# Kernel optimization log

Measured on AMD Instinct MI355X. Metric: run time of the kernel, lower is better.

The kernel has to match this reference:

```python
import jax, jax.numpy as jnp
import numpy as np

N, IN_DIM, KEY_DIM, K, VAL_DIM = 100000, 512, 100, 8, 64


def setup_inputs() -> dict:
    key = jax.random.key(0)
    ks = jax.random.split(key, 7)
    s = 0.02
    return {
        "x": jax.random.normal(ks[0], (N, IN_DIM), dtype=jnp.float32),
        "Wk": jax.random.normal(ks[1], (KEY_DIM, IN_DIM), dtype=jnp.float32) * s,
        "bk": jax.random.normal(ks[2], (KEY_DIM,), dtype=jnp.float32) * s,
        "Wq": jax.random.normal(ks[3], (K, KEY_DIM), dtype=jnp.float32) * s,
        "bq": jax.random.normal(ks[4], (K,), dtype=jnp.float32) * s,
        "Wv": jax.random.normal(ks[5], (VAL_DIM, IN_DIM), dtype=jnp.float32) * s,
        "bv": jax.random.normal(ks[6], (VAL_DIM,), dtype=jnp.float32) * s,
    }


def reference(x, Wk, bk, Wq, bq, Wv, bv):
    # torch.nn.Linear: y = x @ W.T + b
    key = x @ Wk.T + bk                  # [N, key_dim]
    val = x @ Wv.T + bv                  # [N, val_dim]
    que = key @ Wq.T + bq                # [N, k]
    # att_norm == 'softmax': per-sample softmax over the k groups
    w = jax.nn.softmax(que, axis=-1)     # [N, k]
    # per-sample outer product w_i^T @ val_i -> [N, k, val_dim]
    x_group = w[:, :, None] * val[:, None, :]
    return x_group
```

## Files before the change

kernel.cpp:

```cpp
#include <hip/hip_runtime.h>

#define NROWS 100000
#define IN_DIM 512

typedef __attribute__((ext_vector_type(8))) short short8;
typedef __attribute__((ext_vector_type(4))) float f32x4;
typedef unsigned int u32;
typedef const __attribute__((address_space(1))) u32* gptr_t;
typedef __attribute__((address_space(3))) u32* lptr_t;

__device__ inline unsigned short f2bf(float f) {
    union { float f; unsigned u; } v; v.f = f;
    unsigned u = v.u;
    return (unsigned short)((u + 0x7FFFu + ((u >> 16) & 1u)) >> 16);
}

__global__ void qg_prepack(const float* __restrict__ Wk, const float* __restrict__ bk,
                           const float* __restrict__ Wq, const float* __restrict__ bq,
                           const float* __restrict__ Wv,
                           unsigned short* __restrict__ Bp, float* __restrict__ qb) {
    int id = blockIdx.x * 256 + threadIdx.x;
    if (id < 8) {
        float s = bq[id];
        #pragma unroll 4
        for (int j = 0; j < 100; ++j) s += Wq[id * 100 + j] * bk[j];
        qb[id] = s;
    }
    if (id >= 5120) return;
    int lane = id & 63;
    int ks = (id >> 6) & 15;
    int t = id >> 10;
    int c = t * 16 + (lane & 15);
    int kk = ks * 32 + (lane >> 4) * 8;
    short8 pk;
    #pragma unroll
    for (int e = 0; e < 8; ++e) {
        int k2 = kk + e;
        float w;
        if (c < 64) {
            w = Wv[c * IN_DIM + k2];
        } else if (c < 72) {
            float s = 0.f;
            #pragma unroll 4
            for (int j = 0; j < 100; ++j) s += Wq[(c - 64) * 100 + j] * Wk[j * IN_DIM + k2];
            w = s;
        } else {
            w = 0.f;
        }
        pk[e] = (short)f2bf(w);
    }
    ((short8*)Bp)[id] = pk;
}

__global__ __launch_bounds__(128, 1) void qg_main(const float* __restrict__ x,
                                                  const float* __restrict__ bv,
                                                  const unsigned short* __restrict__ Bp,
                                                  const float* __restrict__ qb,
                                                  float* __restrict__ out) {
    __shared__ float smem[36864];
    const int tid = threadIdx.x;
    const int w = tid >> 6;
    const int lane = tid & 63;
    const int g = lane >> 4;
    const int cl = lane & 15;
    const int rowbase = (blockIdx.x * 2 + w) * 16;

    float* Bls = smem;
    float* tile = smem + 20480 + w * 8192;

    float bvr[4];
    #pragma unroll
    for (int t = 0; t < 4; ++t) bvr[t] = bv[t * 16 + cl];
    float qbr = qb[cl & 7];
    asm volatile("s_waitcnt vmcnt(0)" ::: "memory");

    #pragma unroll
    for (int j = 0; j < 40; ++j) {
        const int slot = w * 2560 + j * 64;
        const char* src = (const char*)Bp + ((size_t)(slot + lane)) * 16;
        __builtin_amdgcn_global_load_lds((gptr_t)(const void*)src,
                                         (lptr_t)(void*)(Bls + (size_t)slot * 4), 16, 0, 0);
    }
    __builtin_amdgcn_sched_barrier(0);

    #pragma unroll
    for (int i = 0; i < 32; ++i) {
        const int row = i >> 1;
        const int c = (((i & 1) * 64) + lane) ^ (row & 7);
        const float* src = x + (size_t)(rowbase + row) * IN_DIM + c * 4;
        __builtin_amdgcn_global_load_lds((gptr_t)(const void*)src,
                                         (lptr_t)(void*)(tile + i * 256), 16, 0, 0);
    }
    __builtin_amdgcn_sched_barrier(0);

    asm volatile("s_waitcnt vmcnt(32)" ::: "memory");
    __builtin_amdgcn_s_barrier();
    asm volatile("s_waitcnt vmcnt(0)" ::: "memory");
    __builtin_amdgcn_sched_barrier(0);

    f32x4 acc[5];
    #pragma unroll
    for (int t = 0; t < 5; ++t) acc[t] = (f32x4){0.f, 0.f, 0.f, 0.f};
    const float4* t4 = (const float4*)tile;
    const short8* b8 = (const short8*)Bls;

    #pragma unroll
    for (int s = 0; s < 16; ++s) {
        const int c0 = (s * 8 + g * 2)     ^ (cl & 7);
        const int c1 = (s * 8 + g * 2 + 1) ^ (cl & 7);
        float4 f0 = t4[cl * 128 + c0];
        float4 f1 = t4[cl * 128 + c1];
        short8 af;
        af[0] = (short)f2bf(f0.x); af[1] = (short)f2bf(f0.y);
        af[2] = (short)f2bf(f0.z); af[3] = (short)f2bf(f0.w);
        af[4] = (short)f2bf(f1.x); af[5] = (short)f2bf(f1.y);
        af[6] = (short)f2bf(f1.z); af[7] = (short)f2bf(f1.w);
        #pragma unroll
        for (int t = 0; t < 5; ++t)
            acc[t] = __builtin_amdgcn_mfma_f32_16x16x32_bf16(af, b8[(t * 16 + s) * 64 + lane], acc[t], 0, 0, 0);
    }

    asm volatile("s_waitcnt lgkmcnt(0)" ::: "memory");
    float (*vld)[68] = (float(*)[68])tile;
    float (*wld)[8]  = (float(*)[8])(tile + 16 * 68);
    #pragma unroll
    for (int t = 0; t < 4; ++t) {
        #pragma unroll
        for (int r = 0; r < 4; ++r)
            vld[g * 4 + r][t * 16 + cl] = acc[t][r] + bvr[t];
    }
    if (cl < 8) {
        #pragma unroll
        for (int r = 0; r < 4; ++r)
            wld[g * 4 + r][cl] = acc[4][r] + qbr;
    }
    asm volatile("s_waitcnt lgkmcnt(0)" ::: "memory");

    if (lane < 16) {
        float q[8];
        float m = -1e30f;
        #pragma unroll
        for (int k = 0; k < 8; ++k) { q[k] = wld[lane][k]; m = fmaxf(m, q[k]); }
        float ssum = 0.f;
        #pragma unroll
        for (int k = 0; k < 8; ++k) { q[k] = __expf(q[k] - m); ssum += q[k]; }
        float inv = 1.f / ssum;
        #pragma unroll
        for (int k = 0; k < 8; ++k) wld[lane][k] = q[k] * inv;
    }
    asm volatile("s_waitcnt lgkmcnt(0)" ::: "memory");

    f32x4* outp = (f32x4*)out + (size_t)rowbase * 128;
    #pragma unroll
    for (int it = 0; it < 32; ++it) {
        int idx = it * 64 + lane;
        int row = idx >> 7;
        int j = idx & 127;
        float wgt = wld[row][j >> 4];
        float4 vv = *(const float4*)&vld[row][(j & 15) * 4];
        f32x4 o;
        o[0] = wgt * vv.x; o[1] = wgt * vv.y; o[2] = wgt * vv.z; o[3] = wgt * vv.w;
        __builtin_nontemporal_store(o, &outp[(size_t)row * 128 + j]);
    }
}

extern "C" void kernel_launch(void* const* d_in, const int* in_sizes, int n_in,
                              void* d_out, int out_size, void* d_ws, size_t ws_size,
                              hipStream_t stream) {
    const float* x  = (const float*)d_in[0];
    const float* Wk = (const float*)d_in[1];
    const float* bk = (const float*)d_in[2];
    const float* Wq = (const float*)d_in[3];
    const float* bq = (const float*)d_in[4];
    const float* Wv = (const float*)d_in[5];
    const float* bv = (const float*)d_in[6];
    float* out = (float*)d_out;

    unsigned short* Bp = (unsigned short*)d_ws;
    float* qb = (float*)((char*)d_ws + 81920);

    qg_prepack<<<20, 256, 0, stream>>>(Wk, bk, Wq, bq, Wv, Bp, qb);
    qg_main<<<3125, 128, 0, stream>>>(x, bv, Bp, qb, out);
}
```

Baseline: 120.9 us.

## Make main kernel persistent with atomic tile scheduling and a five-slot load ring

Replaces the one-shot grid of 3125 two-wave blocks with 256 persistent four-wave blocks. Each wave pulls 16-row tiles from a global atomic counter that the prepack kernel resets. x is streamed through a per-wave five-slot LDS ring of 32-column chunks with counted vmcnt waits, so loads for the next chunks and the next tile overlap the MFMA work and the epilogue stores. The packed weights are loaded into LDS once per block instead of once per small block. In exchange the kernel needs an atomic per tile, has an intricate hand-tuned wait-count schedule, and its occupancy is limited to one large block per CU.

```diff
diff --git a/kernel.cpp b/kernel.cpp
--- a/kernel.cpp
+++ b/kernel.cpp
@@ -2,6 +2,7 @@
 
 #define NROWS 100000
 #define IN_DIM 512
+#define NTILES 6250
 
 typedef __attribute__((ext_vector_type(8))) short short8;
 typedef __attribute__((ext_vector_type(4))) float f32x4;
@@ -18,7 +19,8 @@
 __global__ void qg_prepack(const float* __restrict__ Wk, const float* __restrict__ bk,
                            const float* __restrict__ Wq, const float* __restrict__ bq,
                            const float* __restrict__ Wv,
-                           unsigned short* __restrict__ Bp, float* __restrict__ qb) {
+                           unsigned short* __restrict__ Bp, float* __restrict__ qb,
+                           u32* __restrict__ ctr) {
     int id = blockIdx.x * 256 + threadIdx.x;
     if (id < 8) {
         float s = bq[id];
@@ -26,6 +28,7 @@
         for (int j = 0; j < 100; ++j) s += Wq[id * 100 + j] * bk[j];
         qb[id] = s;
     }
+    if (id == 8) *ctr = 0u;
     if (id >= 5120) return;
     int lane = id & 63;
     int ks = (id >> 6) & 15;
@@ -52,21 +55,20 @@
     ((short8*)Bp)[id] = pk;
 }
 
-__global__ __launch_bounds__(128, 1) void qg_main(const float* __restrict__ x,
+__global__ __launch_bounds__(256, 1) void qg_main(const float* __restrict__ x,
                                                   const float* __restrict__ bv,
                                                   const unsigned short* __restrict__ Bp,
                                                   const float* __restrict__ qb,
+                                                  u32* __restrict__ ctr,
                                                   float* __restrict__ out) {
-    __shared__ float smem[36864];
+    __shared__ float Bls[20480];
+    __shared__ float ring[4][2560];
+    __shared__ float epi[4][1216];
     const int tid = threadIdx.x;
     const int w = tid >> 6;
     const int lane = tid & 63;
     const int g = lane >> 4;
     const int cl = lane & 15;
-    const int rowbase = (blockIdx.x * 2 + w) * 16;
-
-    float* Bls = smem;
-    float* tile = smem + 20480 + w * 8192;
 
     float bvr[4];
     #pragma unroll
@@ -74,94 +76,151 @@
     float qbr = qb[cl & 7];
     asm volatile("s_waitcnt vmcnt(0)" ::: "memory");
 
+    int t0 = 0, t1 = 0;
+    if (lane == 0) { t0 = (int)atomicAdd(ctr, 1u); t1 = (int)atomicAdd(ctr, 1u); }
+    int cur = __shfl(t0, 0);
+    int nxt = __shfl(t1, 0);
+
     #pragma unroll
-    for (int j = 0; j < 40; ++j) {
-        const int slot = w * 2560 + j * 64;
-        const char* src = (const char*)Bp + ((size_t)(slot + lane)) * 16;
-        __builtin_amdgcn_global_load_lds((gptr_t)(const void*)src,
-                                         (lptr_t)(void*)(Bls + (size_t)slot * 4), 16, 0, 0);
-    }
-    __builtin_amdgcn_sched_barrier(0);
-
-    #pragma unroll
-    for (int i = 0; i < 32; ++i) {
-        const int row = i >> 1;
-        const int c = (((i & 1) * 64) + lane) ^ (row & 7);
-        const float* src = x + (size_t)(rowbase + row) * IN_DIM + c * 4;
-        __builtin_amdgcn_global_load_lds((gptr_t)(const void*)src,
-                                         (lptr_t)(void*)(tile + i * 256), 16, 0, 0);
-    }
-    __builtin_amdgcn_sched_barrier(0);
-
-    asm volatile("s_waitcnt vmcnt(32)" ::: "memory");
+    for (int j = 0; j < 20; ++j) {
+        int s16 = w * 1280 + j * 64;
+        __builtin_amdgcn_global_load_lds(
+            (gptr_t)(const void*)((const char*)Bp + ((size_t)s16 + lane) * 16),
+            (lptr_t)(void*)(Bls + (size_t)s16 * 4), 16, 0, 0);
+    }
+
+    auto issue_chunk = [&](int rb, int st, int slot) {
+        #pragma unroll
+        for (int l = 0; l < 2; ++l) {
+            int S16 = l * 64 + lane;
+            int row = S16 >> 3;
+            int c = (S16 & 7) ^ (row & 7);
+            const float* src = x + (size_t)(rb + row) * IN_DIM + st * 32 + c * 4;
+            __builtin_amdgcn_global_load_lds((gptr_t)(const void*)src,
+                (lptr_t)(void*)(ring[w] + slot * 512 + l * 256), 16, 0, 0);
+        }
+    };
+
+    {
+        const int rb0 = cur * 16;
+        #pragma unroll
+        for (int s = 0; s < 5; ++s) issue_chunk(rb0, s, s);
+    }
+    asm volatile("s_waitcnt vmcnt(10)" ::: "memory");
     __builtin_amdgcn_s_barrier();
-    asm volatile("s_waitcnt vmcnt(0)" ::: "memory");
-    __builtin_amdgcn_sched_barrier(0);
-
-    f32x4 acc[5];
-    #pragma unroll
-    for (int t = 0; t < 5; ++t) acc[t] = (f32x4){0.f, 0.f, 0.f, 0.f};
-    const float4* t4 = (const float4*)tile;
+
     const short8* b8 = (const short8*)Bls;
-
-    #pragma unroll
-    for (int s = 0; s < 16; ++s) {
-        const int c0 = (s * 8 + g * 2)     ^ (cl & 7);
-        const int c1 = (s * 8 + g * 2 + 1) ^ (cl & 7);
-        float4 f0 = t4[cl * 128 + c0];
-        float4 f1 = t4[cl * 128 + c1];
-        short8 af;
-        af[0] = (short)f2bf(f0.x); af[1] = (short)f2bf(f0.y);
-        af[2] = (short)f2bf(f0.z); af[3] = (short)f2bf(f0.w);
-        af[4] = (short)f2bf(f1.x); af[5] = (short)f2bf(f1.y);
-        af[6] = (short)f2bf(f1.z); af[7] = (short)f2bf(f1.w);
-        #pragma unroll
-        for (int t = 0; t < 5; ++t)
-            acc[t] = __builtin_amdgcn_mfma_f32_16x16x32_bf16(af, b8[(t * 16 + s) * 64 + lane], acc[t], 0, 0, 0);
-    }
-
-    asm volatile("s_waitcnt lgkmcnt(0)" ::: "memory");
-    float (*vld)[68] = (float(*)[68])tile;
-    float (*wld)[8]  = (float(*)[8])(tile + 16 * 68);
-    #pragma unroll
-    for (int t = 0; t < 4; ++t) {
-        #pragma unroll
-        for (int r = 0; r < 4; ++r)
-            vld[g * 4 + r][t * 16 + cl] = acc[t][r] + bvr[t];
-    }
-    if (cl < 8) {
-        #pragma unroll
-        for (int r = 0; r < 4; ++r)
-            wld[g * 4 + r][cl] = acc[4][r] + qbr;
-    }
-    asm volatile("s_waitcnt lgkmcnt(0)" ::: "memory");
-
-    if (lane < 16) {
-        float q[8];
-        float m = -1e30f;
-        #pragma unroll
-        for (int k = 0; k < 8; ++k) { q[k] = wld[lane][k]; m = fmaxf(m, q[k]); }
-        float ssum = 0.f;
-        #pragma unroll
-        for (int k = 0; k < 8; ++k) { q[k] = __expf(q[k] - m); ssum += q[k]; }
-        float inv = 1.f / ssum;
-        #pragma unroll
-        for (int k = 0; k < 8; ++k) wld[lane][k] = q[k] * inv;
-    }
-    asm volatile("s_waitcnt lgkmcnt(0)" ::: "memory");
-
-    f32x4* outp = (f32x4*)out + (size_t)rowbase * 128;
-    #pragma unroll
-    for (int it = 0; it < 32; ++it) {
-        int idx = it * 64 + lane;
-        int row = idx >> 7;
-        int j = idx & 127;
-        float wgt = wld[row][j >> 4];
-        float4 vv = *(const float4*)&vld[row][(j & 15) * 4];
-        f32x4 o;
-        o[0] = wgt * vv.x; o[1] = wgt * vv.y; o[2] = wgt * vv.z; o[3] = wgt * vv.w;
-        __builtin_nontemporal_store(o, &outp[(size_t)row * 128 + j]);
-    }
+    int r0 = 0;
+
+#define CSTEP(S, NW, RBI, STI, DI) do {                                        \
+    asm volatile("s_waitcnt vmcnt(" NW ")" ::: "memory");                      \
+    __builtin_amdgcn_sched_barrier(0);                                         \
+    {                                                                          \
+        const int slot_ = (r0 + (S)) % 5;                                      \
+        const float4* a4_ = (const float4*)(ring[w] + slot_ * 512);            \
+        float4 f0_ = a4_[cl * 8 + ((g * 2) ^ (cl & 7))];                       \
+        float4 f1_ = a4_[cl * 8 + ((g * 2 + 1) ^ (cl & 7))];                   \
+        short8 af_;                                                            \
+        af_[0] = (short)f2bf(f0_.x); af_[1] = (short)f2bf(f0_.y);              \
+        af_[2] = (short)f2bf(f0_.z); af_[3] = (short)f2bf(f0_.w);              \
+        af_[4] = (short)f2bf(f1_.x); af_[5] = (short)f2bf(f1_.y);              \
+        af_[6] = (short)f2bf(f1_.z); af_[7] = (short)f2bf(f1_.w);              \
+        acc[0] = __builtin_amdgcn_mfma_f32_16x16x32_bf16(af_, b8[(0 * 16 + (S)) * 64 + lane], acc[0], 0, 0, 0); \
+        acc[1] = __builtin_amdgcn_mfma_f32_16x16x32_bf16(af_, b8[(1 * 16 + (S)) * 64 + lane], acc[1], 0, 0, 0); \
+        acc[2] = __builtin_amdgcn_mfma_f32_16x16x32_bf16(af_, b8[(2 * 16 + (S)) * 64 + lane], acc[2], 0, 0, 0); \
+        acc[3] = __builtin_amdgcn_mfma_f32_16x16x32_bf16(af_, b8[(3 * 16 + (S)) * 64 + lane], acc[3], 0, 0, 0); \
+        acc[4] = __builtin_amdgcn_mfma_f32_16x16x32_bf16(af_, b8[(4 * 16 + (S)) * 64 + lane], acc[4], 0, 0, 0); \
+        asm volatile("s_waitcnt lgkmcnt(0)" ::: "memory");                     \
+        __builtin_amdgcn_sched_barrier(0);                                     \
+        if (DI) issue_chunk((RBI), (STI), slot_);                              \
+    }                                                                          \
+} while (0)
+
+#define TILE16(L04) do {                                                       \
+    const int rbc_ = cur * 16;                                                 \
+    const int rbn_ = nxt * 16;                                                 \
+    const bool hn_ = (nxt < NTILES);                                           \
+    CSTEP(0,  L04, rbc_, 5,  true);                                            \
+    CSTEP(1,  L04, rbc_, 6,  true);                                            \
+    CSTEP(2,  L04, rbc_, 7,  true);                                            \
+    CSTEP(3,  L04, rbc_, 8,  true);                                            \
+    CSTEP(4,  L04, rbc_, 9,  true);                                            \
+    CSTEP(5,  "8", rbc_, 10, true);                                            \
+    CSTEP(6,  "8", rbc_, 11, true);                                            \
+    CSTEP(7,  "8", rbc_, 12, true);                                            \
+    CSTEP(8,  "8", rbc_, 13, true);                                            \
+    CSTEP(9,  "8", rbc_, 14, true);                                            \
+    CSTEP(10, "8", rbc_, 15, true);                                            \
+    CSTEP(11, "8", rbn_, 0,  hn_);                                             \
+    CSTEP(12, "8", rbn_, 1,  hn_);                                             \
+    CSTEP(13, "8", rbn_, 2,  hn_);                                             \
+    CSTEP(14, "8", rbn_, 3,  hn_);                                             \
+    CSTEP(15, "8", rbn_, 4,  hn_);                                             \
+} while (0)
+
+    float* vld = epi[w];
+    float* wld = epi[w] + 16 * 68;
+
+    bool first = true;
+    while (cur < NTILES) {
+        int ta = 0;
+        if (lane == 0) ta = (int)atomicAdd(ctr, 1u);
+        int aft = __shfl(ta, 0);
+
+        f32x4 acc[5];
+        #pragma unroll
+        for (int t = 0; t < 5; ++t) acc[t] = (f32x4){0.f, 0.f, 0.f, 0.f};
+
+        if (first) { TILE16("8"); } else { TILE16("40"); }
+
+        const int rb = cur * 16;
+        #pragma unroll
+        for (int t = 0; t < 4; ++t) {
+            #pragma unroll
+            for (int r = 0; r < 4; ++r)
+                vld[(g * 4 + r) * 68 + t * 16 + cl] = acc[t][r] + bvr[t];
+        }
+        if (cl < 8) {
+            #pragma unroll
+            for (int r = 0; r < 4; ++r)
+                wld[(g * 4 + r) * 8 + cl] = acc[4][r] + qbr;
+        }
+        asm volatile("s_waitcnt lgkmcnt(0)" ::: "memory");
+
+        if (lane < 16) {
+            float q[8];
+            float m = -1e30f;
+            #pragma unroll
+            for (int k = 0; k < 8; ++k) { q[k] = wld[lane * 8 + k]; m = fmaxf(m, q[k]); }
+            float ssum = 0.f;
+            #pragma unroll
+            for (int k = 0; k < 8; ++k) { q[k] = __expf(q[k] - m); ssum += q[k]; }
+            float inv = 1.f / ssum;
+            #pragma unroll
+            for (int k = 0; k < 8; ++k) wld[lane * 8 + k] = q[k] * inv;
+        }
+        asm volatile("s_waitcnt lgkmcnt(0)" ::: "memory");
+
+        f32x4* outp = (f32x4*)out + (size_t)rb * 128;
+        #pragma unroll
+        for (int it = 0; it < 32; ++it) {
+            int idx = it * 64 + lane;
+            int row = idx >> 7;
+            int j = idx & 127;
+            float wgt = wld[row * 8 + (j >> 4)];
+            float4 vv = *(const float4*)&vld[row * 68 + (j & 15) * 4];
+            f32x4 o;
+            o[0] = wgt * vv.x; o[1] = wgt * vv.y; o[2] = wgt * vv.z; o[3] = wgt * vv.w;
+            __builtin_nontemporal_store(o, &outp[(size_t)row * 128 + j]);
+        }
+
+        r0 = (r0 == 4) ? 0 : (r0 + 1);
+        cur = nxt;
+        nxt = aft;
+        first = false;
+    }
+#undef TILE16
+#undef CSTEP
 }
 
 extern "C" void kernel_launch(void* const* d_in, const int* in_sizes, int n_in,
@@ -178,7 +237,8 @@
 
     unsigned short* Bp = (unsigned short*)d_ws;
     float* qb = (float*)((char*)d_ws + 81920);
-
-    qg_prepack<<<20, 256, 0, stream>>>(Wk, bk, Wq, bq, Wv, Bp, qb);
-    qg_main<<<3125, 128, 0, stream>>>(x, bv, Bp, qb, out);
-}
+    u32* ctr = (u32*)((char*)d_ws + 81984);
+
+    qg_prepack<<<20, 256, 0, stream>>>(Wk, bk, Wq, bq, Wv, Bp, qb, ctr);
+    qg_main<<<256, 256, 0, stream>>>(x, bv, Bp, qb, ctr, out);
+}
```

New measurement: 150.7 us. +24.6%, slower.
